# Kernel tuning notes

Measured on AMD Instinct MI355X. Metric: run time of the kernel, lower is better.

## Reference

```python
import jax, jax.numpy as jnp
import numpy as np

B, S, HID = 2, 2048, 1024
H, KV, D = 8, 4, 128
GROUPS = H // KV
SCALE = D ** -0.5
ROPE_THETA = 10000.0


def _rope_tables(seq_len, dim):
    inv = 1.0 / (ROPE_THETA ** (jnp.arange(0, dim, 2, dtype=jnp.float32) / dim))
    t = jnp.arange(seq_len, dtype=jnp.float32)
    freqs = jnp.outer(t, inv)                          # [S, D/2]
    emb = jnp.concatenate([freqs, freqs], axis=-1)     # [S, D]
    return jnp.cos(emb), jnp.sin(emb)


def _rotate_half(x):
    x1, x2 = jnp.split(x, 2, axis=-1)
    return jnp.concatenate([-x2, x1], axis=-1)


def setup_inputs() -> dict:
    key = jax.random.key(0)
    ks = jax.random.split(key, 7)
    std = 0.02
    hidden = jax.random.normal(ks[0], (B, S, HID), jnp.float32)
    Wq = jax.random.normal(ks[1], (HID, H * D), jnp.float32) * std
    Wk = jax.random.normal(ks[2], (HID, KV * D), jnp.float32) * std
    Wv = jax.random.normal(ks[3], (HID, KV * D), jnp.float32) * std
    Wdt = jax.random.normal(ks[4], (KV * D, H), jnp.float32) * std
    A = jax.random.normal(ks[5], (H,), jnp.float32) * 0.1
    Wo = jax.random.normal(ks[6], (H * D, HID), jnp.float32) * std
    cos, sin = _rope_tables(S, D)
    causal_mask = jnp.triu(jnp.ones((S, S), jnp.int32), 1)[None, None]  # 1 = masked
    return dict(hidden=hidden, Wq=Wq, Wk=Wk, Wv=Wv, Wdt=Wdt, A=A, Wo=Wo,
                cos=cos, sin=sin, causal_mask=causal_mask)


def reference(hidden, Wq, Wk, Wv, Wdt, A, Wo, cos, sin, causal_mask):
    # q/k/v projections -> [B, heads, S, D]
    q = (hidden @ Wq).reshape(B, S, H, D).transpose(0, 2, 1, 3)
    k = (hidden @ Wk).reshape(B, S, KV, D).transpose(0, 2, 1, 3)
    v = (hidden @ Wv).reshape(B, S, KV, D).transpose(0, 2, 1, 3)
    # RoPE
    c = cos[None, None]  # [1,1,S,D]
    s = sin[None, None]
    q = q * c + _rotate_half(q) * s
    k = k * c + _rotate_half(k) * s
    # dynamic mask: dt_proj over flattened per-position value states
    v_flat = v.transpose(0, 2, 1, 3).reshape(B, S, KV * D)
    dt = v_flat @ Wdt                                        # [B, S, H]
    dyn = jnp.exp(A[None, None, :] * jax.nn.softplus(dt))    # [B, S, H]
    attn_bias = dyn.transpose(0, 2, 1)[:, :, None, :]        # [B, H, 1, kv]
    min_val = jnp.finfo(jnp.float32).min
    attn_bias = jnp.where(causal_mask != 0, min_val, attn_bias)  # [B, H, S, S]
    # GQA repeat of kv heads
    k_rep = jnp.repeat(k, GROUPS, axis=1)
    v_rep = jnp.repeat(v, GROUPS, axis=1)
    scores = jnp.einsum('bhqd,bhkd->bhqk', q, k_rep) * SCALE + attn_bias
    w = jax.nn.softmax(scores.astype(jnp.float32), axis=-1).astype(hidden.dtype)
    out = jnp.einsum('bhqk,bhkd->bhqd', w, v_rep)
    out = out.transpose(0, 2, 1, 3).reshape(B, S, H * D)
    return out @ Wo
```

## Files before the change

kernel.cpp:

```cpp
#include <hip/hip_runtime.h>

typedef unsigned short u16;
typedef unsigned int   u32;
typedef __bf16 bf16;
typedef bf16  bf16x8 __attribute__((ext_vector_type(8)));
typedef float f32x4  __attribute__((ext_vector_type(4)));

#define S_LEN 2048
#define SCALE 0.08838834764831845f
#define SMAX  8.0f

__device__ __forceinline__ float bf2f(u16 u) {
  union { u32 i; float f; } v; v.i = ((u32)u) << 16; return v.f;
}
__device__ __forceinline__ u16 f2b(float f) {
  union { float f; u32 i; } v; v.f = f;
  u32 x = v.i;
  u32 r = x + 0x7fffu + ((x >> 16) & 1u);
  return (u16)(r >> 16);
}
__device__ __forceinline__ float2 bfpair(u32 u) {
  union { u32 i; float f; } lo, hi;
  lo.i = u << 16; hi.i = u & 0xffff0000u;
  float2 r; r.x = lo.f; r.y = hi.f; return r;
}

__device__ __forceinline__ void gl_lds16(const u16* g, u16* l) {
  __builtin_amdgcn_global_load_lds(
      (const __attribute__((address_space(1))) void*)g,
      (__attribute__((address_space(3))) void*)l, 16, 0, 0);
}

__device__ __forceinline__ void load16(const float* p, u16* dst) {
  #pragma unroll
  for (int i = 0; i < 16; i += 4) {
    float4 v = *(const float4*)(p + i);
    dst[i]     = f2b(v.x); dst[i + 1] = f2b(v.y);
    dst[i + 2] = f2b(v.z); dst[i + 3] = f2b(v.w);
  }
}

__device__ __forceinline__ void storeo(float* p, float v) { *p = v; }
__device__ __forceinline__ void storeo(u16* p, float v)   { *p = f2b(v); }

__device__ __forceinline__ bf16x8 frag8(const u16* p) {
  union { uint4 u; bf16x8 v; } c;
  c.u = *(const uint4*)p;
  return c.v;
}
__device__ __forceinline__ f32x4 zero4() {
  f32x4 z = {0.f, 0.f, 0.f, 0.f}; return z;
}

__global__ __launch_bounds__(256) void prep_kernel(
    const float* __restrict__ H, u16* __restrict__ HB,
    const float* __restrict__ Wq, const float* __restrict__ Wk,
    const float* __restrict__ Wv, const float* __restrict__ Wo,
    u16* __restrict__ Wqt, u16* __restrict__ Wkt,
    u16* __restrict__ Wvt, u16* __restrict__ Wot)
{
  const int bid = blockIdx.x;
  if (bid < 2048) {
    const size_t base = ((size_t)bid * 256 + threadIdx.x) * 8;
    float4 a = *(const float4*)(H + base);
    float4 b = *(const float4*)(H + base + 4);
    u16 tmp[8];
    tmp[0]=f2b(a.x); tmp[1]=f2b(a.y); tmp[2]=f2b(a.z); tmp[3]=f2b(a.w);
    tmp[4]=f2b(b.x); tmp[5]=f2b(b.y); tmp[6]=f2b(b.z); tmp[7]=f2b(b.w);
    *(uint4*)(HB + base) = *(uint4*)tmp;
    return;
  }
  const int b2 = bid - 2048;
  const float* src; u16* dst; int N, ko, no;
  if (b2 < 256)      { src = Wq; dst = Wqt; N = 1024; int q = b2;       ko = (q >> 4) * 64; no = (q & 15) * 64; }
  else if (b2 < 384) { src = Wk; dst = Wkt; N = 512;  int q = b2 - 256; ko = (q >> 3) * 64; no = (q & 7) * 64; }
  else if (b2 < 512) { src = Wv; dst = Wvt; N = 512;  int q = b2 - 384; ko = (q >> 3) * 64; no = (q & 7) * 64; }
  else               { src = Wo; dst = Wot; N = 1024; int q = b2 - 512; ko = (q >> 4) * 64; no = (q & 15) * 64; }

  __shared__ __align__(16) u16 T[64][68];
  const int t = threadIdx.x;
  const int r = t >> 2, c = (t & 3) * 16;
  {
    u16 tmp[16];
    load16(src + (size_t)(ko + r) * N + no + c, tmp);
    *(uint4*)&T[r][c]     = *(uint4*)tmp;
    *(uint4*)&T[r][c + 8] = *(uint4*)(tmp + 8);
  }
  __syncthreads();
  {
    u16 tmp[16];
    #pragma unroll
    for (int j = 0; j < 16; ++j) tmp[j] = T[c + j][r];
    u16* o = dst + (size_t)(no + r) * 1024 + ko + c;
    *(uint4*)o       = *(uint4*)tmp;
    *(uint4*)(o + 8) = *(uint4*)(tmp + 8);
  }
}

__global__ __launch_bounds__(256) void gemm3(
    const u16* __restrict__ A, int lda, int Kdim,
    const u16* __restrict__ W0, u16* __restrict__ O0, int ldo0,
    const u16* __restrict__ W1, u16* __restrict__ O1, int ldo1,
    const u16* __restrict__ W2, u16* __restrict__ O2, int ldo2,
    int c1, int c2,
    const float* __restrict__ cosb, const float* __restrict__ sinb, int ropeLim)
{
  const int flat = blockIdx.y * gridDim.x + blockIdx.x;
  const int xcd = flat & 7, rr = flat >> 3;
  const int bx = ((xcd & 1) << 3) + (rr & 7);
  const int by = ((xcd >> 1) << 3) + (rr >> 3);
  const int n0 = bx * 128;
  const int m0 = by * 128;
  const u16* W; u16* O; int ldo, col;
  if (n0 < c1)      { W = W0; O = O0; ldo = ldo0; col = n0; }
  else if (n0 < c2) { W = W1; O = O1; ldo = ldo1; col = n0 - c1; }
  else              { W = W2; O = O2; ldo = ldo2; col = n0 - c2; }
  const bool doRope = (n0 < ropeLim);

  __shared__ __align__(16) u16 As[128 * 64];
  __shared__ __align__(16) u16 Bs[128 * 64];

  const int t    = threadIdx.x;
  const int w    = t >> 6, lane = t & 63, quad = lane >> 4, l16 = lane & 15;
  const int sw   = l16 & 7;
  const int srow = lane >> 3;
  const int schk = (lane & 7) ^ srow;
  int kcs[2];
  #pragma unroll
  for (int ks = 0; ks < 2; ++ks) kcs[ks] = ((ks * 4 + quad) ^ sw) * 8;

  const u16* Ag = A + (size_t)(m0 + w * 32 + srow) * lda + schk * 8;
  const u16* Bg = W + (size_t)(col + w * 32 + srow) * Kdim + schk * 8;

  f32x4 acc[2][8];
  #pragma unroll
  for (int i2 = 0; i2 < 2; ++i2)
    #pragma unroll
    for (int nt = 0; nt < 8; ++nt) acc[i2][nt] = zero4();

  for (int k0 = 0; k0 < Kdim; k0 += 64) {
    __syncthreads();
    #pragma unroll
    for (int j = 0; j < 4; ++j) {
      gl_lds16(Ag + (size_t)(j * 8) * lda + k0, &As[(w * 4 + j) * 512]);
      gl_lds16(Bg + (size_t)(j * 8) * Kdim + k0, &Bs[(w * 4 + j) * 512]);
    }
    __syncthreads();
    #pragma unroll
    for (int ks = 0; ks < 2; ++ks) {
      bf16x8 a0 = frag8(&As[(w * 32 + l16) * 64 + kcs[ks]]);
      bf16x8 a1 = frag8(&As[(w * 32 + 16 + l16) * 64 + kcs[ks]]);
      #pragma unroll
      for (int nt = 0; nt < 8; ++nt) {
        bf16x8 bw = frag8(&Bs[(nt * 16 + l16) * 64 + kcs[ks]]);
        acc[0][nt] = __builtin_amdgcn_mfma_f32_16x16x32_bf16(a0, bw, acc[0][nt], 0, 0, 0);
        acc[1][nt] = __builtin_amdgcn_mfma_f32_16x16x32_bf16(a1, bw, acc[1][nt], 0, 0, 0);
      }
    }
  }

  if (doRope) {
    #pragma unroll
    for (int i2 = 0; i2 < 2; ++i2)
      #pragma unroll
      for (int r = 0; r < 4; ++r) {
        const int m = m0 + w * 32 + i2 * 16 + quad * 4 + r;
        const int sp_ = m & (S_LEN - 1);
        const float* cp = cosb + (size_t)sp_ * 128;
        const float* sp = sinb + (size_t)sp_ * 128;
        #pragma unroll
        for (int nt = 0; nt < 4; ++nt) {
          const int d = nt * 16 + l16;
          const float a  = acc[i2][nt][r];
          const float bb = acc[i2][nt + 4][r];
          acc[i2][nt][r]     = a * cp[d]       - bb * sp[d];
          acc[i2][nt + 4][r] = bb * cp[d + 64] + a * sp[d + 64];
        }
      }
  }

  #pragma unroll
  for (int i2 = 0; i2 < 2; ++i2)
    #pragma unroll
    for (int nt = 0; nt < 8; ++nt)
      #pragma unroll
      for (int r = 0; r < 4; ++r) {
        const int m = m0 + w * 32 + i2 * 16 + quad * 4 + r;
        const int n = col + nt * 16 + l16;
        O[(size_t)m * ldo + n] = f2b(acc[i2][nt][r]);
      }
}

template <typename TO>
__global__ __launch_bounds__(256) void gemm2(
    const u16* __restrict__ A, int lda, int Kdim,
    const u16* __restrict__ W0, TO* __restrict__ O0, int ldo0,
    const u16* __restrict__ W1, TO* __restrict__ O1, int ldo1,
    const u16* __restrict__ W2, TO* __restrict__ O2, int ldo2,
    int c1, int c2)
{
  const int flat = blockIdx.y * gridDim.x + blockIdx.x;
  const int xcd = flat & 7, rr = flat >> 3;
  const int bx = ((xcd & 1) << 3) + (rr & 7);
  const int by = ((xcd >> 1) << 3) + (rr >> 3);
  const int n0 = bx * 64;
  const int m0 = by * 128;
  const u16* W; TO* O; int ldo, col;
  if (n0 < c1)      { W = W0; O = O0; ldo = ldo0; col = n0; }
  else if (n0 < c2) { W = W1; O = O1; ldo = ldo1; col = n0 - c1; }
  else              { W = W2; O = O2; ldo = ldo2; col = n0 - c2; }

  __shared__ __align__(16) u16 As[128 * 64];
  __shared__ __align__(16) u16 Bs[64 * 64];

  const int t    = threadIdx.x;
  const int w    = t >> 6, lane = t & 63, quad = lane >> 4, l16 = lane & 15;
  const int sw   = l16 & 7;
  const int srow = lane >> 3;
  const int schk = (lane & 7) ^ srow;
  int kcs[2];
  #pragma unroll
  for (int ks = 0; ks < 2; ++ks) kcs[ks] = ((ks * 4 + quad) ^ sw) * 8;

  const u16* Ag = A + (size_t)(m0 + w * 32 + srow) * lda + schk * 8;
  const u16* Bg = W + (size_t)(col + w * 16 + srow) * Kdim + schk * 8;

  f32x4 acc[2][4];
  #pragma unroll
  for (int i2 = 0; i2 < 2; ++i2)
    #pragma unroll
    for (int nt = 0; nt < 4; ++nt) acc[i2][nt] = zero4();

  for (int k0 = 0; k0 < Kdim; k0 += 64) {
    __syncthreads();
    #pragma unroll
    for (int j = 0; j < 4; ++j)
      gl_lds16(Ag + (size_t)(j * 8) * lda + k0, &As[(w * 4 + j) * 512]);
    #pragma unroll
    for (int j = 0; j < 2; ++j)
      gl_lds16(Bg + (size_t)(j * 8) * Kdim + k0, &Bs[(w * 2 + j) * 512]);
    __syncthreads();
    #pragma unroll
    for (int ks = 0; ks < 2; ++ks) {
      bf16x8 a0 = frag8(&As[(w * 32 + l16) * 64 + kcs[ks]]);
      bf16x8 a1 = frag8(&As[(w * 32 + 16 + l16) * 64 + kcs[ks]]);
      #pragma unroll
      for (int nt = 0; nt < 4; ++nt) {
        bf16x8 bw = frag8(&Bs[(nt * 16 + l16) * 64 + kcs[ks]]);
        acc[0][nt] = __builtin_amdgcn_mfma_f32_16x16x32_bf16(a0, bw, acc[0][nt], 0, 0, 0);
        acc[1][nt] = __builtin_amdgcn_mfma_f32_16x16x32_bf16(a1, bw, acc[1][nt], 0, 0, 0);
      }
    }
  }
  #pragma unroll
  for (int i2 = 0; i2 < 2; ++i2)
    #pragma unroll
    for (int nt = 0; nt < 4; ++nt)
      #pragma unroll
      for (int r = 0; r < 4; ++r) {
        const int m = m0 + w * 32 + i2 * 16 + quad * 4 + r;
        const int n = col + nt * 16 + l16;
        storeo(O + (size_t)m * ldo + n, acc[i2][nt][r]);
      }
}

__global__ __launch_bounds__(256) void dyn_kernel(const u16* __restrict__ Vb, const float* __restrict__ Wdt,
                                                  const float* __restrict__ Af, float* __restrict__ dynT)
{
  __shared__ __align__(16) float Wl[4096];
  const int t = threadIdx.x;
  #pragma unroll
  for (int i = 0; i < 4; ++i)
    *(float4*)&Wl[(t + i * 256) * 4] = *(const float4*)(Wdt + (t + i * 256) * 4);
  __syncthreads();

  const int wid = t >> 6, lane = t & 63;
  const int pos = blockIdx.x * 4 + wid;
  float acc[8];
  #pragma unroll
  for (int h = 0; h < 8; ++h) acc[h] = 0.f;
  for (int j = lane; j < 512; j += 64) {
    float v = bf2f(Vb[(size_t)pos * 512 + j]);
    float4 w0 = *(const float4*)&Wl[j * 8];
    float4 w1 = *(const float4*)&Wl[j * 8 + 4];
    acc[0] += v * w0.x; acc[1] += v * w0.y; acc[2] += v * w0.z; acc[3] += v * w0.w;
    acc[4] += v * w1.x; acc[5] += v * w1.y; acc[6] += v * w1.z; acc[7] += v * w1.w;
  }
  #pragma unroll
  for (int off = 32; off > 0; off >>= 1)
    #pragma unroll
    for (int h = 0; h < 8; ++h) acc[h] += __shfl_down(acc[h], off, 64);
  if (lane == 0) {
    const int b = pos >> 11, s = pos & (S_LEN - 1);
    #pragma unroll
    for (int h = 0; h < 8; ++h) {
      float dt = acc[h];
      float sp = (dt > 20.f) ? dt : log1pf(__expf(dt));
      dynT[(size_t)(b * 8 + h) * S_LEN + s] = __expf(Af[h] * sp);
    }
  }
}

__global__ __launch_bounds__(256) void vtrans_kernel(const u16* __restrict__ Vb, u16* __restrict__ VTg)
{
  const int sx = blockIdx.x, kvh = blockIdx.y, b = blockIdx.z;
  __shared__ __align__(16) u16 T[64][132];
  const int t = threadIdx.x;
  {
    const int r = t >> 2, c = (t & 3) * 32;
    const u16* src = Vb + (size_t)(b * S_LEN + sx * 64 + r) * 512 + kvh * 128 + c;
    #pragma unroll
    for (int i = 0; i < 4; ++i)
      *(uint4*)&T[r][c + i * 8] = *(const uint4*)(src + i * 8);
  }
  __syncthreads();
  {
    const int d = t >> 1, cs = (t & 1) * 32;
    u16* dst = VTg + ((size_t)((b * 4 + kvh) * 128 + d)) * S_LEN + sx * 64 + cs;
    #pragma unroll
    for (int i = 0; i < 4; ++i) {
      u16 tmp[8];
      #pragma unroll
      for (int j = 0; j < 8; ++j) tmp[j] = T[cs + i * 8 + j][d];
      *(uint4*)(dst + i * 8) = *(uint4*)tmp;
    }
  }
}

__global__ __launch_bounds__(256, 3) void attn_mfma(const u16* __restrict__ Qb, const u16* __restrict__ Kb,
                                                    const u16* __restrict__ VTg, const float* __restrict__ dynT,
                                                    u16* __restrict__ ctx,
                                                    u16* __restrict__ PO, float* __restrict__ PL)
{
  const int idx = blockIdx.x;
  const int g = (idx & 7) | (((idx >> 3) & 1) << 3);
  const int b = g >> 3, h = g & 7, kvh = h >> 1;
  const int fp = 79 - (idx >> 4);
  int s, c;
  if (fp < 8)       { s = fp; c = 0; }
  else if (fp < 24) { s = 8 + ((fp - 8) >> 1);  c = (fp - 8) & 1; }
  else if (fp < 48) { int r2 = fp - 24; int q3 = r2 / 3; s = 16 + q3; c = r2 - q3 * 3; }
  else              { s = 24 + ((fp - 48) >> 2); c = (fp - 48) & 3; }
  const int q0  = s * 64;
  const int kt0 = c * 8;
  const int kt1 = (c == (s >> 3)) ? s : (kt0 + 7);

  __shared__ __align__(16) u16 Ks[64 * 128];
  __shared__ __align__(16) u16 Vs[128 * 64];
  __shared__ __align__(16) u16 Ps[4][16 * 64];

  const int t = threadIdx.x;
  const int wid = t >> 6, lane = t & 63, quad = lane >> 4, l16 = lane & 15;
  const int sw = l16 & 7;

  int kcs[4];
  #pragma unroll
  for (int ks = 0; ks < 4; ++ks) kcs[ks] = ((ks * 4 + quad) ^ sw) * 8;

  const u16* KgL[4];
  const u16* VgL[4];
  #pragma unroll
  for (int j = 0; j < 4; ++j) {
    const int krj = (wid * 4 + j) * 4 + (lane >> 4);
    const int kcj = (lane & 15) ^ (((j & 1) << 2) + (lane >> 4));
    KgL[j] = Kb + (size_t)(b * S_LEN + krj) * 512 + kvh * 128 + kcj * 8;
    const int vrj = (wid * 4 + j) * 8 + (lane >> 3);
    const int vcj = (lane & 7) ^ (lane >> 3);
    VgL[j] = VTg + ((size_t)((b * 4 + kvh) * 128 + vrj)) * S_LEN + vcj * 8;
  }

  bf16x8 qf[4];
  {
    const u16* qrow = Qb + (size_t)(b * S_LEN + q0 + wid * 16 + l16) * 1024 + h * 128 + quad * 8;
    #pragma unroll
    for (int ks = 0; ks < 4; ++ks) qf[ks] = frag8(qrow + ks * 32);
  }

  const float* dynbase = dynT + (size_t)(b * 8 + h) * S_LEN + l16;

  f32x4 accO[8];
  #pragma unroll
  for (int nt = 0; nt < 8; ++nt) accO[nt] = zero4();
  float l_lane[4] = {0.f, 0.f, 0.f, 0.f};

  for (int kt = kt0; kt <= kt1; ++kt) {
    const int k0 = kt * 64;
    __syncthreads();
    #pragma unroll
    for (int j = 0; j < 4; ++j)
      gl_lds16(KgL[j] + (size_t)k0 * 512, &Ks[(wid * 4 + j) * 512]);
    #pragma unroll
    for (int j = 0; j < 4; ++j)
      gl_lds16(VgL[j] + k0, &Vs[(wid * 4 + j) * 512]);
    float dv[4];
    #pragma unroll
    for (int nt = 0; nt < 4; ++nt) dv[nt] = dynbase[k0 + nt * 16];
    __syncthreads();

    f32x4 accS[4];
    #pragma unroll
    for (int nt = 0; nt < 4; ++nt) accS[nt] = zero4();
    __builtin_amdgcn_s_setprio(1);
    #pragma unroll
    for (int ks = 0; ks < 4; ++ks)
      #pragma unroll
      for (int nt = 0; nt < 4; ++nt)
        accS[nt] = __builtin_amdgcn_mfma_f32_16x16x32_bf16(
            qf[ks], frag8(&Ks[(nt * 16 + l16) * 128 + kcs[ks]]), accS[nt], 0, 0, 0);
    __builtin_amdgcn_s_setprio(0);

    if (kt < s) {
      #pragma unroll
      for (int nt = 0; nt < 4; ++nt)
        #pragma unroll
        for (int r = 0; r < 4; ++r) {
          float p = __expf(fmaf(accS[nt][r], SCALE, dv[nt]) - SMAX);
          l_lane[r] += p;
          const int prow = quad * 4 + r;
          Ps[wid][prow * 64 + (((nt * 2 + (l16 >> 3)) ^ (prow & 7)) << 3) + sw] = f2b(p);
        }
    } else {
      const int qq = wid * 16 + quad * 4;
      #pragma unroll
      for (int nt = 0; nt < 4; ++nt) {
        const int kk = nt * 16 + l16;
        #pragma unroll
        for (int r = 0; r < 4; ++r) {
          float p = (kk > qq + r) ? 0.f
                    : __expf(fmaf(accS[nt][r], SCALE, dv[nt]) - SMAX);
          l_lane[r] += p;
          const int prow = quad * 4 + r;
          Ps[wid][prow * 64 + (((nt * 2 + (l16 >> 3)) ^ (prow & 7)) << 3) + sw] = f2b(p);
        }
      }
    }

    __builtin_amdgcn_s_setprio(1);
    #pragma unroll
    for (int ks = 0; ks < 2; ++ks) {
      bf16x8 a = frag8(&Ps[wid][l16 * 64 + kcs[ks]]);
      #pragma unroll
      for (int nt = 0; nt < 8; ++nt)
        accO[nt] = __builtin_amdgcn_mfma_f32_16x16x32_bf16(
            a, frag8(&Vs[(nt * 16 + l16) * 64 + kcs[ks]]), accO[nt], 0, 0, 0);
    }
    __builtin_amdgcn_s_setprio(0);
  }

  #pragma unroll
  for (int off = 1; off < 16; off <<= 1)
    #pragma unroll
    for (int r = 0; r < 4; ++r) l_lane[r] += __shfl_xor(l_lane[r], off, 64);

  if (s < 8) {
    float linv[4];
    #pragma unroll
    for (int r = 0; r < 4; ++r) linv[r] = 1.f / l_lane[r];
    #pragma unroll
    for (int nt = 0; nt < 8; ++nt)
      #pragma unroll
      for (int r = 0; r < 4; ++r) {
        const int qq = q0 + wid * 16 + quad * 4 + r;
        const int d  = nt * 16 + l16;
        ctx[(size_t)(b * S_LEN + qq) * 1024 + h * 128 + d] = f2b(accO[nt][r] * linv[r]);
      }
  } else {
    const int slot = g * 72 + (fp - 8);
    u16 tmp[32];
    #pragma unroll
    for (int nt = 0; nt < 8; ++nt)
      #pragma unroll
      for (int r = 0; r < 4; ++r) tmp[nt * 4 + r] = f2b(accO[nt][r]);
    u16* po = PO + (size_t)slot * 8192 + wid * 2048 + lane * 32;
    #pragma unroll
    for (int i = 0; i < 4; ++i) *(uint4*)(po + i * 8) = *(uint4*)(tmp + i * 8);
    if (l16 == 0) {
      #pragma unroll
      for (int r = 0; r < 4; ++r) PL[slot * 64 + wid * 16 + quad * 4 + r] = l_lane[r];
    }
  }
}

__global__ __launch_bounds__(256) void attn_combine(const u16* __restrict__ PO, const float* __restrict__ PL,
                                                    u16* __restrict__ ctx)
{
  const int s = 8 + (int)blockIdx.x;
  const int g = (int)blockIdx.y;
  const int b = g >> 3, h = g & 7;
  const int g2 = s >> 3;
  const int nch = g2 + 1;
  const int base = (g2 == 1) ? 8 : (g2 == 2) ? 24 : 48;
  const int slot0 = g * 72 + base + (s - g2 * 8) * nch - 8;
  const int t = threadIdx.x;
  const int wid = t >> 6, lane = t & 63, quad = lane >> 4, l16 = lane & 15;

  float acc[32];
  #pragma unroll
  for (int i = 0; i < 32; ++i) acc[i] = 0.f;
  float ls[4] = {0.f, 0.f, 0.f, 0.f};

  for (int cth = 0; cth < nch; ++cth) {
    const u16* po = PO + (size_t)(slot0 + cth) * 8192 + wid * 2048 + lane * 32;
    #pragma unroll
    for (int i = 0; i < 4; ++i) {
      uint4 v = *(const uint4*)(po + i * 8);
      u32 u[4] = {v.x, v.y, v.z, v.w};
      #pragma unroll
      for (int j = 0; j < 4; ++j) {
        float2 p = bfpair(u[j]);
        acc[i * 8 + 2 * j]     += p.x;
        acc[i * 8 + 2 * j + 1] += p.y;
      }
    }
    #pragma unroll
    for (int r = 0; r < 4; ++r) ls[r] += PL[(slot0 + cth) * 64 + wid * 16 + quad * 4 + r];
  }

  float linv[4];
  #pragma unroll
  for (int r = 0; r < 4; ++r) linv[r] = 1.f / ls[r];
  #pragma unroll
  for (int nt = 0; nt < 8; ++nt)
    #pragma unroll
    for (int r = 0; r < 4; ++r) {
      const int qq = s * 64 + wid * 16 + quad * 4 + r;
      const int d  = nt * 16 + l16;
      ctx[(size_t)(b * S_LEN + qq) * 1024 + h * 128 + d] = f2b(acc[nt * 4 + r] * linv[r]);
    }
}

extern "C" void kernel_launch(void* const* d_in, const int* in_sizes, int n_in,
                              void* d_out, int out_size, void* d_ws, size_t ws_size,
                              hipStream_t stream)
{
  const float* hidden = (const float*)d_in[0];
  const float* Wq     = (const float*)d_in[1];
  const float* Wk     = (const float*)d_in[2];
  const float* Wv     = (const float*)d_in[3];
  const float* Wdt    = (const float*)d_in[4];
  const float* Af     = (const float*)d_in[5];
  const float* Wo     = (const float*)d_in[6];
  const float* cosb   = (const float*)d_in[7];
  const float* sinb   = (const float*)d_in[8];
  float* out = (float*)d_out;

  u16* Qb  = (u16*)d_ws;
  u16* Kb  = Qb + (size_t)4096 * 1024;
  u16* Vb  = Kb + (size_t)4096 * 512;
  u16* VTg = Vb + (size_t)4096 * 512;
  float* dynT = (float*)(VTg + (size_t)4096 * 512);
  u16* PO = (u16*)(dynT + (size_t)16 * S_LEN);
  float* PL = (float*)(PO + (size_t)16 * 72 * 8192);
  u16* HB  = (u16*)(PL + (size_t)16 * 72 * 64);
  u16* Wqt = HB  + (size_t)4096 * 1024;
  u16* Wkt = Wqt + (size_t)1024 * 1024;
  u16* Wvt = Wkt + (size_t)512 * 1024;
  u16* Wot = Wvt + (size_t)512 * 1024;
  u16* ctx = Qb;

  prep_kernel<<<2816, 256, 0, stream>>>(hidden, HB, Wq, Wk, Wv, Wo, Wqt, Wkt, Wvt, Wot);
  gemm3<<<dim3(16, 32), 256, 0, stream>>>(HB, 1024, 1024,
      Wqt, Qb, 1024,
      Wkt, Kb,  512,
      Wvt, Vb,  512,
      1024, 1536,
      cosb, sinb, 1536);
  dyn_kernel<<<1024, 256, 0, stream>>>(Vb, Wdt, Af, dynT);
  vtrans_kernel<<<dim3(32, 4, 2), 256, 0, stream>>>(Vb, VTg);
  attn_mfma<<<1280, 256, 0, stream>>>(Qb, Kb, VTg, dynT, ctx, PO, PL);
  attn_combine<<<dim3(24, 16), 256, 0, stream>>>(PO, PL, ctx);
  gemm2<float><<<dim3(16, 32), 256, 0, stream>>>(ctx, 1024, 1024,
      Wot, out, 1024,
      Wot, out, 1024,
      Wot, out, 1024,
      1 << 30, 1 << 30);
}
```

Measured before the change: 213.9 us.

## Double-buffer GEMM LDS loads, fuse V transpose into QKV GEMM, reswizzle P

Both GEMM kernels now use two LDS buffers, prefetching the next K tile while MFMAs run on the current one, and drop one barrier per iteration. The QKV GEMM also writes the transposed V directly from its accumulators, which removes the separate vtrans kernel launch and its extra read and write of V. The attention kernel's P tile in shared memory gets a new XOR swizzle intended to reduce bank conflicts on both the writes and the fragment reads. In exchange, LDS use doubles, which may lower occupancy, and the transposed V stores are narrow 8-byte strided writes. The prefetch issued right after the single barrier depends on gl_lds16 completion being waited for at the next barrier.

```diff
diff --git a/kernel.cpp b/kernel.cpp
--- a/kernel.cpp
+++ b/kernel.cpp
@@ -103,7 +103,8 @@
     const u16* __restrict__ W1, u16* __restrict__ O1, int ldo1,
     const u16* __restrict__ W2, u16* __restrict__ O2, int ldo2,
     int c1, int c2,
-    const float* __restrict__ cosb, const float* __restrict__ sinb, int ropeLim)
+    const float* __restrict__ cosb, const float* __restrict__ sinb, int ropeLim,
+    u16* __restrict__ VTg)
 {
   const int flat = blockIdx.y * gridDim.x + blockIdx.x;
   const int xcd = flat & 7, rr = flat >> 3;
@@ -116,9 +117,10 @@
   else if (n0 < c2) { W = W1; O = O1; ldo = ldo1; col = n0 - c1; }
   else              { W = W2; O = O2; ldo = ldo2; col = n0 - c2; }
   const bool doRope = (n0 < ropeLim);
-
-  __shared__ __align__(16) u16 As[128 * 64];
-  __shared__ __align__(16) u16 Bs[128 * 64];
+  const bool isV    = (n0 >= c2);
+
+  __shared__ __align__(16) u16 As[2][128 * 64];
+  __shared__ __align__(16) u16 Bs[2][128 * 64];
 
   const int t    = threadIdx.x;
   const int w    = t >> 6, lane = t & 63, quad = lane >> 4, l16 = lane & 15;
@@ -138,21 +140,29 @@
     #pragma unroll
     for (int nt = 0; nt < 8; ++nt) acc[i2][nt] = zero4();
 
-  for (int k0 = 0; k0 < Kdim; k0 += 64) {
+  #pragma unroll
+  for (int j = 0; j < 4; ++j) {
+    gl_lds16(Ag + (size_t)(j * 8) * lda, &As[0][(w * 4 + j) * 512]);
+    gl_lds16(Bg + (size_t)(j * 8) * Kdim, &Bs[0][(w * 4 + j) * 512]);
+  }
+
+  int cur = 0;
+  for (int k0 = 0; k0 < Kdim; k0 += 64, cur ^= 1) {
     __syncthreads();
-    #pragma unroll
-    for (int j = 0; j < 4; ++j) {
-      gl_lds16(Ag + (size_t)(j * 8) * lda + k0, &As[(w * 4 + j) * 512]);
-      gl_lds16(Bg + (size_t)(j * 8) * Kdim + k0, &Bs[(w * 4 + j) * 512]);
-    }
-    __syncthreads();
+    if (k0 + 64 < Kdim) {
+      #pragma unroll
+      for (int j = 0; j < 4; ++j) {
+        gl_lds16(Ag + (size_t)(j * 8) * lda + k0 + 64, &As[cur ^ 1][(w * 4 + j) * 512]);
+        gl_lds16(Bg + (size_t)(j * 8) * Kdim + k0 + 64, &Bs[cur ^ 1][(w * 4 + j) * 512]);
+      }
+    }
     #pragma unroll
     for (int ks = 0; ks < 2; ++ks) {
-      bf16x8 a0 = frag8(&As[(w * 32 + l16) * 64 + kcs[ks]]);
-      bf16x8 a1 = frag8(&As[(w * 32 + 16 + l16) * 64 + kcs[ks]]);
+      bf16x8 a0 = frag8(&As[cur][(w * 32 + l16) * 64 + kcs[ks]]);
+      bf16x8 a1 = frag8(&As[cur][(w * 32 + 16 + l16) * 64 + kcs[ks]]);
       #pragma unroll
       for (int nt = 0; nt < 8; ++nt) {
-        bf16x8 bw = frag8(&Bs[(nt * 16 + l16) * 64 + kcs[ks]]);
+        bf16x8 bw = frag8(&Bs[cur][(nt * 16 + l16) * 64 + kcs[ks]]);
         acc[0][nt] = __builtin_amdgcn_mfma_f32_16x16x32_bf16(a0, bw, acc[0][nt], 0, 0, 0);
         acc[1][nt] = __builtin_amdgcn_mfma_f32_16x16x32_bf16(a1, bw, acc[1][nt], 0, 0, 0);
       }
@@ -189,6 +199,22 @@
         const int n = col + nt * 16 + l16;
         O[(size_t)m * ldo + n] = f2b(acc[i2][nt][r]);
       }
+
+  if (isV) {
+    #pragma unroll
+    for (int i2 = 0; i2 < 2; ++i2)
+      #pragma unroll
+      for (int nt = 0; nt < 8; ++nt) {
+        const int m = m0 + w * 32 + i2 * 16 + quad * 4;
+        const int bb_ = m >> 11, ss = m & (S_LEN - 1);
+        const int d = col + nt * 16 + l16;
+        u16 tmp4[4];
+        #pragma unroll
+        for (int r = 0; r < 4; ++r) tmp4[r] = f2b(acc[i2][nt][r]);
+        u16* dst = VTg + ((size_t)((bb_ * 4 + (d >> 7)) * 128 + (d & 127))) * S_LEN + ss;
+        *(uint2*)dst = *(const uint2*)tmp4;
+      }
+  }
 }
 
 template <typename TO>
@@ -210,8 +236,8 @@
   else if (n0 < c2) { W = W1; O = O1; ldo = ldo1; col = n0 - c1; }
   else              { W = W2; O = O2; ldo = ldo2; col = n0 - c2; }
 
-  __shared__ __align__(16) u16 As[128 * 64];
-  __shared__ __align__(16) u16 Bs[64 * 64];
+  __shared__ __align__(16) u16 As[2][128 * 64];
+  __shared__ __align__(16) u16 Bs[2][64 * 64];
 
   const int t    = threadIdx.x;
   const int w    = t >> 6, lane = t & 63, quad = lane >> 4, l16 = lane & 15;
@@ -231,22 +257,31 @@
     #pragma unroll
     for (int nt = 0; nt < 4; ++nt) acc[i2][nt] = zero4();
 
-  for (int k0 = 0; k0 < Kdim; k0 += 64) {
+  #pragma unroll
+  for (int j = 0; j < 4; ++j)
+    gl_lds16(Ag + (size_t)(j * 8) * lda, &As[0][(w * 4 + j) * 512]);
+  #pragma unroll
+  for (int j = 0; j < 2; ++j)
+    gl_lds16(Bg + (size_t)(j * 8) * Kdim, &Bs[0][(w * 2 + j) * 512]);
+
+  int cur = 0;
+  for (int k0 = 0; k0 < Kdim; k0 += 64, cur ^= 1) {
     __syncthreads();
-    #pragma unroll
-    for (int j = 0; j < 4; ++j)
-      gl_lds16(Ag + (size_t)(j * 8) * lda + k0, &As[(w * 4 + j) * 512]);
-    #pragma unroll
-    for (int j = 0; j < 2; ++j)
-      gl_lds16(Bg + (size_t)(j * 8) * Kdim + k0, &Bs[(w * 2 + j) * 512]);
-    __syncthreads();
+    if (k0 + 64 < Kdim) {
+      #pragma unroll
+      for (int j = 0; j < 4; ++j)
+        gl_lds16(Ag + (size_t)(j * 8) * lda + k0 + 64, &As[cur ^ 1][(w * 4 + j) * 512]);
+      #pragma unroll
+      for (int j = 0; j < 2; ++j)
+        gl_lds16(Bg + (size_t)(j * 8) * Kdim + k0 + 64, &Bs[cur ^ 1][(w * 2 + j) * 512]);
+    }
     #pragma unroll
     for (int ks = 0; ks < 2; ++ks) {
-      bf16x8 a0 = frag8(&As[(w * 32 + l16) * 64 + kcs[ks]]);
-      bf16x8 a1 = frag8(&As[(w * 32 + 16 + l16) * 64 + kcs[ks]]);
+      bf16x8 a0 = frag8(&As[cur][(w * 32 + l16) * 64 + kcs[ks]]);
+      bf16x8 a1 = frag8(&As[cur][(w * 32 + 16 + l16) * 64 + kcs[ks]]);
       #pragma unroll
       for (int nt = 0; nt < 4; ++nt) {
-        bf16x8 bw = frag8(&Bs[(nt * 16 + l16) * 64 + kcs[ks]]);
+        bf16x8 bw = frag8(&Bs[cur][(nt * 16 + l16) * 64 + kcs[ks]]);
         acc[0][nt] = __builtin_amdgcn_mfma_f32_16x16x32_bf16(a0, bw, acc[0][nt], 0, 0, 0);
         acc[1][nt] = __builtin_amdgcn_mfma_f32_16x16x32_bf16(a1, bw, acc[1][nt], 0, 0, 0);
       }
@@ -297,32 +332,6 @@
       float dt = acc[h];
       float sp = (dt > 20.f) ? dt : log1pf(__expf(dt));
       dynT[(size_t)(b * 8 + h) * S_LEN + s] = __expf(Af[h] * sp);
-    }
-  }
-}
-
-__global__ __launch_bounds__(256) void vtrans_kernel(const u16* __restrict__ Vb, u16* __restrict__ VTg)
-{
-  const int sx = blockIdx.x, kvh = blockIdx.y, b = blockIdx.z;
-  __shared__ __align__(16) u16 T[64][132];
-  const int t = threadIdx.x;
-  {
-    const int r = t >> 2, c = (t & 3) * 32;
-    const u16* src = Vb + (size_t)(b * S_LEN + sx * 64 + r) * 512 + kvh * 128 + c;
-    #pragma unroll
-    for (int i = 0; i < 4; ++i)
-      *(uint4*)&T[r][c + i * 8] = *(const uint4*)(src + i * 8);
-  }
-  __syncthreads();
-  {
-    const int d = t >> 1, cs = (t & 1) * 32;
-    u16* dst = VTg + ((size_t)((b * 4 + kvh) * 128 + d)) * S_LEN + sx * 64 + cs;
-    #pragma unroll
-    for (int i = 0; i < 4; ++i) {
-      u16 tmp[8];
-      #pragma unroll
-      for (int j = 0; j < 8; ++j) tmp[j] = T[cs + i * 8 + j][d];
-      *(uint4*)(dst + i * 8) = *(uint4*)tmp;
     }
   }
 }
@@ -353,9 +362,12 @@
   const int wid = t >> 6, lane = t & 63, quad = lane >> 4, l16 = lane & 15;
   const int sw = l16 & 7;
 
-  int kcs[4];
+  int kcs[4], pcs[2];
   #pragma unroll
   for (int ks = 0; ks < 4; ++ks) kcs[ks] = ((ks * 4 + quad) ^ sw) * 8;
+  const int phr = sw ^ ((l16 >> 3) << 1);
+  #pragma unroll
+  for (int ks = 0; ks < 2; ++ks) pcs[ks] = ((ks * 4 + quad) ^ phr) * 8;
 
   const u16* KgL[4];
   const u16* VgL[4];
@@ -417,7 +429,8 @@
           float p = __expf(fmaf(accS[nt][r], SCALE, dv[nt]) - SMAX);
           l_lane[r] += p;
           const int prow = quad * 4 + r;
-          Ps[wid][prow * 64 + (((nt * 2 + (l16 >> 3)) ^ (prow & 7)) << 3) + sw] = f2b(p);
+          const int ph = (prow & 7) ^ ((prow >> 3) << 1);
+          Ps[wid][prow * 64 + (((nt * 2 + (l16 >> 3)) ^ ph) << 3) + sw] = f2b(p);
         }
     } else {
       const int qq = wid * 16 + quad * 4;
@@ -430,7 +443,8 @@
                     : __expf(fmaf(accS[nt][r], SCALE, dv[nt]) - SMAX);
           l_lane[r] += p;
           const int prow = quad * 4 + r;
-          Ps[wid][prow * 64 + (((nt * 2 + (l16 >> 3)) ^ (prow & 7)) << 3) + sw] = f2b(p);
+          const int ph = (prow & 7) ^ ((prow >> 3) << 1);
+          Ps[wid][prow * 64 + (((nt * 2 + (l16 >> 3)) ^ ph) << 3) + sw] = f2b(p);
         }
       }
     }
@@ -438,7 +452,7 @@
     __builtin_amdgcn_s_setprio(1);
     #pragma unroll
     for (int ks = 0; ks < 2; ++ks) {
-      bf16x8 a = frag8(&Ps[wid][l16 * 64 + kcs[ks]]);
+      bf16x8 a = frag8(&Ps[wid][l16 * 64 + pcs[ks]]);
       #pragma unroll
       for (int nt = 0; nt < 8; ++nt)
         accO[nt] = __builtin_amdgcn_mfma_f32_16x16x32_bf16(
@@ -564,9 +578,8 @@
       Wkt, Kb,  512,
       Wvt, Vb,  512,
       1024, 1536,
-      cosb, sinb, 1536);
+      cosb, sinb, 1536, VTg);
   dyn_kernel<<<1024, 256, 0, stream>>>(Vb, Wdt, Af, dynT);
-  vtrans_kernel<<<dim3(32, 4, 2), 256, 0, stream>>>(Vb, VTg);
   attn_mfma<<<1280, 256, 0, stream>>>(Qb, Kb, VTg, dynT, ctx, PO, PL);
   attn_combine<<<dim3(24, 16), 256, 0, stream>>>(PO, PL, ctx);
   gemm2<float><<<dim3(16, 32), 256, 0, stream>>>(ctx, 1024, 1024,
```

Measured after the change: 206.5 us. 1.04x faster.
